# Kernel tuning notes

Hardware: AMD Instinct MI355X
Metric: run time of the kernel (lower is better)

## Reference

```python
import jax, jax.numpy as jnp
import numpy as np

WINDOW = 2048
STEP = WINDOW // 2                 # 1024
N_SAMPLES = 131072
N_COEFFS = WINDOW // 2 + 1         # 1025
N_FRAMES = N_SAMPLES // STEP       # 128
Z_DIM = 128
BATCH, N_EVENTS, IMP_SAMPLES = 64, 1, 4096
BASE_RES = 0.02
RES_RANGE = (1.0 - BASE_RES) * 0.99


def setup_inputs() -> dict:
    key = jax.random.key(0)
    k1, k2, k3 = jax.random.split(key, 3)
    z = jax.random.normal(k1, (BATCH, N_EVENTS, Z_DIM), dtype=jnp.float32)
    impulse = jax.random.normal(k2, (BATCH, N_EVENTS, IMP_SAMPLES), dtype=jnp.float32)
    # stand-in for ConvUpsample: linear z -> (n_coeffs * n_frames)
    W_tf = jax.random.normal(k3, (Z_DIM, N_COEFFS * N_FRAMES), dtype=jnp.float32) * 0.02
    b_tf = jnp.zeros((N_COEFFS * N_FRAMES,), dtype=jnp.float32)
    return {"z": z, "impulse": impulse, "W_tf": W_tf, "b_tf": b_tf}


def _hann(n):
    # periodic hann (torch.hann_window default)
    return (0.5 - 0.5 * jnp.cos(2.0 * jnp.pi * jnp.arange(n) / n)).astype(jnp.float32)


def reference(z, impulse, W_tf, b_tf):
    B, E, imp_len = impulse.shape
    pad = N_SAMPLES - imp_len + WINDOW
    x = jnp.pad(impulse, ((0, 0), (0, 0), (0, pad)))  # (B,E,n_samples+window)
    win = _hann(WINDOW)

    # windowed_audio: overlapping frames * hann window -> (B,E,F,W)
    idx = jnp.arange(N_FRAMES)[:, None] * STEP + jnp.arange(WINDOW)[None, :]
    windowed = x[..., idx] * win

    # transfer functions: linear, reshape (C,F) -> transpose to (F,C), squash
    tf = (z.reshape(-1, Z_DIM) @ W_tf + b_tf).reshape(B, E, N_COEFFS, N_FRAMES)
    tf = jnp.transpose(tf, (0, 1, 3, 2))                       # (B,E,F,C)
    tf = BASE_RES + jax.nn.sigmoid(tf) * RES_RANGE

    cur_specs = jnp.fft.rfft(windowed, axis=-1)                # (B,E,F,C) complex64

    # advance_one_frame rotation: [re,im] @ [[c,-s],[s,-c]]
    g = jnp.linspace(0.0, np.pi, N_COEFFS).astype(jnp.float32)
    c, s = jnp.cos(g), jnp.sin(g)

    def step(prev_audio, inp):
        cur_spec, tfi = inp
        ps = jnp.fft.rfft(prev_audio, axis=-1)
        re, im = ps.real, ps.imag
        rot = jax.lax.complex(re * c + im * s, -(re * s + im * c))
        spec = (cur_spec + rot) * tfi
        audio = jnp.fft.irfft(spec, n=WINDOW, axis=-1)
        return audio, audio

    xs = (jnp.moveaxis(cur_specs, 2, 0), jnp.moveaxis(tf, 2, 0))
    init = jnp.zeros((B, E, WINDOW), dtype=jnp.float32)  # i==0: zero prev spec
    _, frames = jax.lax.scan(step, init, xs)             # (F,B,E,W)
    frames = jnp.moveaxis(frames, 0, 2) * win            # overlap_add apply_window=True

    # overlap-add with hop = WINDOW//2, vectorized via half-frame reshapes
    first = frames[..., :STEP].reshape(B, E, N_FRAMES * STEP)
    second = frames[..., STEP:].reshape(B, E, N_FRAMES * STEP)
    out = jnp.zeros((B, E, (N_FRAMES + 1) * STEP), dtype=jnp.float32)
    out = out.at[..., : N_FRAMES * STEP].add(first)
    out = out.at[..., STEP:].add(second)
    return out[..., :N_SAMPLES]
```

## Files before the change

### kernel.cpp

```cpp
#include <hip/hip_runtime.h>

#define NB 64
#define ZDIM 128
#define NCOEF 1025
#define NFR 128
#define COLS 131200
#define WINSZ 2048
#define HALFW 1024
#define NSAMP 131072
#define IMPN 4096
#define NCHUNK 32
#define NCK 31

#define TF_OFF   0
#define TF_SZ    (NB*COLS)
#define TFT_OFF  (TF_OFF + TF_SZ)
#define TFT_SZ   (NB*NFR*NCOEF)
#define CUR_OFF  (TFT_OFF + TFT_SZ)
#define CUR_SZ   (NB*4*NCOEF*2)
#define CK_OFF   (CUR_OFF + CUR_SZ)
#define CK_SZ    (NCK*NB*NCOEF*2)
#define WINT_OFF (CK_OFF + CK_SZ)
#define WINT_SZ  (WINSZ)
#define TW_OFF   (WINT_OFF + WINT_SZ)
#define TW_SZ    (HALFW*2)

#define PHYS(i) ((i) ^ (((i) >> 5) & 3))

typedef short bf16x8 __attribute__((ext_vector_type(8)));
typedef float f32x4 __attribute__((ext_vector_type(4)));

__global__ __launch_bounds__(256) void init_tables(float* __restrict__ winT,
                                                   float2* __restrict__ twG) {
  int i = blockIdx.x * 256 + threadIdx.x;
  if (i < WINSZ) {
    winT[i] = 0.5f - 0.5f * cosf((float)(2.0 * 3.14159265358979323846 / 2048.0) * (float)i);
  }
  if (i < HALFW) {
    float ang = (float)(-2.0 * 3.14159265358979323846 / 2048.0) * (float)i;
    float sv, cv;
    sincosf(ang, &sv, &cv);
    twG[i] = make_float2(cv, sv);
  }
}

__device__ __forceinline__ short f2bf(float f) {
  unsigned u = __builtin_bit_cast(unsigned, f);
  u += 0x7FFFu + ((u >> 16) & 1u);
  return (short)(u >> 16);
}

__global__ __launch_bounds__(256) void tf_gemm_mfma(const float* __restrict__ z,
                                                    const float* __restrict__ W,
                                                    const float* __restrict__ bias,
                                                    float* __restrict__ tf) {
  int tid = threadIdx.x;
  int wave = tid >> 6, lane = tid & 63;
  int colw = blockIdx.x * 128 + wave * 32;
  int lr = lane & 15;
  int lk = (lane >> 4) * 8;
  int lq = (lane >> 4) * 4;

  float bv[2];
#pragma unroll
  for (int n = 0; n < 2; ++n) bv[n] = bias[colw + 16 * n + lr];

  f32x4 acc[4][2];
#pragma unroll
  for (int m = 0; m < 4; ++m)
#pragma unroll
    for (int n = 0; n < 2; ++n)
      acc[m][n] = f32x4{bv[n], bv[n], bv[n], bv[n]};

#pragma unroll
  for (int s = 0; s < 4; ++s) {
    int k0 = s * 32 + lk;
    bf16x8 afr[4];
#pragma unroll
    for (int m = 0; m < 4; ++m) {
      const float* zp = z + (size_t)(16 * m + lr) * ZDIM + k0;
      float4 z0 = *reinterpret_cast<const float4*>(zp);
      float4 z1 = *reinterpret_cast<const float4*>(zp + 4);
      afr[m] = bf16x8{f2bf(z0.x), f2bf(z0.y), f2bf(z0.z), f2bf(z0.w),
                      f2bf(z1.x), f2bf(z1.y), f2bf(z1.z), f2bf(z1.w)};
    }
    bf16x8 bfr[2];
#pragma unroll
    for (int n = 0; n < 2; ++n) {
      const float* wp = W + (size_t)k0 * COLS + colw + 16 * n + lr;
      bfr[n] = bf16x8{f2bf(wp[0 * (size_t)COLS]), f2bf(wp[1 * (size_t)COLS]),
                      f2bf(wp[2 * (size_t)COLS]), f2bf(wp[3 * (size_t)COLS]),
                      f2bf(wp[4 * (size_t)COLS]), f2bf(wp[5 * (size_t)COLS]),
                      f2bf(wp[6 * (size_t)COLS]), f2bf(wp[7 * (size_t)COLS])};
    }
#pragma unroll
    for (int m = 0; m < 4; ++m)
#pragma unroll
      for (int n = 0; n < 2; ++n)
        acc[m][n] = __builtin_amdgcn_mfma_f32_16x16x32_bf16(afr[m], bfr[n], acc[m][n], 0, 0, 0);
  }

  const float RESR = (1.0f - 0.02f) * 0.99f;
#pragma unroll
  for (int n = 0; n < 2; ++n) {
    int col = colw + 16 * n + lr;
#pragma unroll
    for (int m = 0; m < 4; ++m) {
      int rowb = 16 * m + lq;
#pragma unroll
      for (int r = 0; r < 4; ++r) {
        float x = acc[m][n][r];
        float sg = 1.0f / (1.0f + __expf(-x));
        tf[(size_t)(rowb + r) * COLS + col] = 0.02f + sg * RESR;
      }
    }
  }
}

static __device__ __forceinline__ void wg_fft2048(float* ar, float* ai,
                                                  float* br, float* bi,
                                                  const float2* tw,
                                                  float** outr, float** outi) {
  float *xr = ar, *xi = ai, *yr = br, *yi = bi;
  int m = 1;
  for (int s = 0; s < 11; ++s) {
    __syncthreads();
#pragma unroll
    for (int it = 0; it < 4; ++it) {
      int t = (int)threadIdx.x + it * 256;
      int jm = t & ~(m - 1);
      float x0r = xr[t], x0i = xi[t];
      float x1r = xr[t + 1024], x1i = xi[t + 1024];
      float2 w = tw[jm];
      float sr = x0r + x1r, si = x0i + x1i;
      float dr = x0r - x1r, di = x0i - x1i;
      float pr = dr * w.x - di * w.y;
      float pi = dr * w.y + di * w.x;
      yr[t + jm] = sr;      yi[t + jm] = si;
      yr[t + jm + m] = pr;  yi[t + jm + m] = pi;
    }
    float* t0 = xr; xr = yr; yr = t0;
    float* t1 = xi; xi = yi; yi = t1;
    m <<= 1;
  }
  __syncthreads();
  *outr = xr; *outi = xi;
}

__global__ __launch_bounds__(256) void fwd_fft_kernel(const float* __restrict__ imp,
                                                      const float* __restrict__ winT,
                                                      const float2* __restrict__ twG,
                                                      float2* __restrict__ cur) {
  __shared__ float b0r[WINSZ], b0i[WINSZ], b1r[WINSZ], b1i[WINSZ];
  __shared__ float2 tw[HALFW];
  int wg = blockIdx.x;
  int b = wg >> 2, f = wg & 3;
  int tid = threadIdx.x;

  for (int i = tid; i < HALFW; i += 256) tw[i] = twG[i];
  for (int w = tid; w < WINSZ; w += 256) {
    int s = f * HALFW + w;
    float v = (s < IMPN) ? imp[(size_t)b * IMPN + s] * winT[w] : 0.0f;
    b0r[w] = v;
    b0i[w] = 0.0f;
  }
  float *rr, *ri;
  wg_fft2048(b0r, b0i, b1r, b1i, tw, &rr, &ri);
  for (int k = tid; k < NCOEF; k += 256)
    cur[(size_t)wg * NCOEF + k] = make_float2(rr[k], ri[k]);
}

__global__ __launch_bounds__(256) void recur_ck_t(const float* __restrict__ tf,
                                                  const float2* __restrict__ cur,
                                                  float2* __restrict__ ckp,
                                                  float* __restrict__ tft) {
  int id = blockIdx.x * 256 + threadIdx.x;
  if (id >= NB * NCOEF) return;
  int b = id / NCOEF;
  int k = id - b * NCOEF;

  float g = 3.14159265358979323846f * (float)k / 1024.0f;
  float sg, cg;
  sincosf(g, &sg, &cg);
  bool herm = (k == 0) || (k == HALFW);

  const float4* tf4 = (const float4*)(tf + (size_t)b * COLS + (size_t)k * NFR);
  const float2* curb = cur + (size_t)b * 4 * NCOEF + k;
  float* tftb = tft + (size_t)b * NFR * NCOEF + k;

  float pre = 0.0f, pim = 0.0f;
  for (int f4 = 0; f4 < 32; ++f4) {
    float4 tv = tf4[f4];
    float tfs[4] = {tv.x, tv.y, tv.z, tv.w};
#pragma unroll
    for (int u = 0; u < 4; ++u) {
      int f = 4 * f4 + u;
      tftb[(size_t)f * NCOEF] = tfs[u];
      if (f < 124) {
        float tfv = tfs[u];
        float cr = 0.0f, ci = 0.0f;
        if (f < 4) {
          float2 cv = curb[(size_t)f * NCOEF];
          cr = cv.x; ci = cv.y;
        }
        float ire = herm ? 0.0f : pim;
        float rre = fmaf(pre, cg, ire * sg);
        float rim = -fmaf(pre, sg, ire * cg);
        float sre = (cr + rre) * tfv;
        float sim = (ci + rim) * tfv;
        if ((f & 3) == 2)
          ckp[(size_t)((f - 2) >> 2) * NB * NCOEF + (size_t)b * NCOEF + k] = make_float2(sre, sim);
        pre = sre; pim = sim;
      }
    }
  }
}

__global__ __launch_bounds__(256) void fused_resyn(const float* __restrict__ tft,
                                                   const float2* __restrict__ cur,
                                                   const float2* __restrict__ ckp,
                                                   const float* __restrict__ winT,
                                                   const float2* __restrict__ twG,
                                                   float* __restrict__ out) {
  __shared__ float L0r[1024], L0i[1024], L1r[1024], L1i[1024];
  __shared__ float2 twL[256];

  int bidx = blockIdx.x;
  int b = bidx >> 5, c = bidx & 31;
  int tid = threadIdx.x;

  twL[tid] = twG[2 * tid];

  float pre[5], pim[5], cgv[5], sgv[5];
#pragma unroll
  for (int i = 0; i < 5; ++i) {
    if (i == 4) { cgv[4] = -1.0f; sgv[4] = 0.0f; }
    else {
      float2 tv = twG[tid + 256 * i];
      cgv[i] = tv.x; sgv[i] = -tv.y;
    }
    pre[i] = 0.0f; pim[i] = 0.0f;
  }
  if (c > 0) {
    const float2* ck = ckp + ((size_t)(c - 1) * NB + b) * NCOEF;
#pragma unroll
    for (int i = 0; i < 5; ++i) {
      if (i == 4 && tid != 0) continue;
      int k = (i == 4) ? 1024 : tid + 256 * i;
      float2 v = ck[k];
      pre[i] = v.x; pim[i] = v.y;
    }
  }

  int fs = (c == 0) ? 0 : 4 * c - 1;
  int fe2 = 4 * c + 3;
  float ce0 = 0.0f, co0 = 0.0f, ce1 = 0.0f, co1 = 0.0f;
  const float* tftb = tft + (size_t)b * NFR * NCOEF;
  const float2* curb = cur + (size_t)b * 4 * NCOEF;
  const float2* win2 = (const float2*)winT;
  const float scale = 1.0f / 1024.0f;
  __syncthreads();

  for (int f = fs; f <= fe2; ++f) {
    const float* tfr = tftb + (size_t)f * NCOEF;
    float sreg[5], simg[5];
#pragma unroll
    for (int i = 0; i < 5; ++i) {
      if (i == 4 && tid != 0) { sreg[4] = 0.0f; simg[4] = 0.0f; continue; }
      int k = (i == 4) ? 1024 : tid + 256 * i;
      float tfv = tfr[k];
      float cr = 0.0f, ci = 0.0f;
      if (f < 4) {
        float2 cv = curb[(size_t)f * NCOEF + k];
        cr = cv.x; ci = cv.y;
      }
      float rre = fmaf(pre[i], cgv[i], pim[i] * sgv[i]);
      float rim = -fmaf(pre[i], sgv[i], pim[i] * cgv[i]);
      float sre = (cr + rre) * tfv;
      float sim = (ci + rim) * tfv;
      sreg[i] = sre; simg[i] = sim;
      pre[i] = sre; pim[i] = sim;
    }
    __syncthreads();
#pragma unroll
    for (int i = 0; i < 4; ++i) {
      int pk = PHYS(tid + 256 * i);
      L1r[pk] = sreg[i]; L1i[pk] = simg[i];
    }
    __syncthreads();
#pragma unroll
    for (int it = 0; it < 4; ++it) {
      int j = tid + it * 256;
      float2 tg = twG[j];
      float cc = tg.x, sn = -tg.y;
      int pj = PHYS(j);
      float xjr = L1r[pj], xji = L1i[pj];
      float xmr, xmi;
      if (j == 0) { xmr = sreg[4]; xmi = 0.0f; }
      else { int pm = PHYS(1024 - j); xmr = L1r[pm]; xmi = L1i[pm]; }
      float Xer = 0.5f * (xjr + xmr), Xei = 0.5f * (xji - xmi);
      float Xpr = 0.5f * (xjr - xmr), Xpi = 0.5f * (xji + xmi);
      float Xor_ = Xpr * cc - Xpi * sn;
      float Xoi_ = Xpr * sn + Xpi * cc;
      L0r[pj] = Xer - Xoi_;
      L0i[pj] = -(Xei + Xor_);
    }
    int t = tid;
#pragma unroll
    for (int st = 0; st < 5; ++st) {
      __syncthreads();
      int s = 1 << (2 * st);
      int q = t & (s - 1);
      int j = t & ~(s - 1);
      float2 w1 = twL[j];
      float w1x = w1.x, w1y = w1.y;
      float w2x = w1x * w1x - w1y * w1y, w2y = 2.0f * w1x * w1y;
      float w3x = w2x * w1x - w2y * w1y, w3y = w2x * w1y + w2y * w1x;
      int i0 = PHYS(t), i1 = PHYS(t + 256), i2 = PHYS(t + 512), i3 = PHYS(t + 768);
      int wb = (j << 2) + q;
      int o0 = PHYS(wb), o1 = PHYS(wb + s), o2 = PHYS(wb + 2 * s), o3 = PHYS(wb + 3 * s);
      const float *xr, *xi;
      float *yr, *yi;
      if (st & 1) { xr = L1r; xi = L1i; yr = L0r; yi = L0i; }
      else        { xr = L0r; xi = L0i; yr = L1r; yi = L1i; }
      float ar_ = xr[i0], ai_ = xi[i0];
      float br_ = xr[i1], bi_ = xi[i1];
      float cr_ = xr[i2], ci_ = xi[i2];
      float dr_ = xr[i3], di_ = xi[i3];
      float apcr = ar_ + cr_, apci = ai_ + ci_;
      float amcr = ar_ - cr_, amci = ai_ - ci_;
      float bpdr = br_ + dr_, bpdi = bi_ + di_;
      float bmdr = br_ - dr_, bmdi = bi_ - di_;
      yr[o0] = apcr + bpdr;             yi[o0] = apci + bpdi;
      float t1r = amcr + bmdi, t1i = amci - bmdr;
      yr[o1] = t1r * w1x - t1i * w1y;   yi[o1] = t1r * w1y + t1i * w1x;
      float t2r = apcr - bpdr, t2i = apci - bpdi;
      yr[o2] = t2r * w2x - t2i * w2y;   yi[o2] = t2r * w2y + t2i * w2x;
      float t3r = amcr - bmdi, t3i = amci + bmdr;
      yr[o3] = t3r * w3x - t3i * w3y;   yi[o3] = t3r * w3y + t3i * w3x;
    }
    __syncthreads();
#pragma unroll
    for (int it = 0; it < 2; ++it) {
      int mI = tid + it * 256;
      float2 wa = win2[mI];
      float2 wb2 = win2[mI + 512];
      int pa = PHYS(mI), pb = PHYS(mI + 512);
      float fe_ = L1r[pa] * scale * wa.x;
      float fo_ = -L1i[pa] * scale * wa.y;
      float se_ = L1r[pb] * scale * wb2.x;
      float so_ = -L1i[pb] * scale * wb2.y;
      if (f >= 4 * c) {
        float2* ob = (float2*)(out + (size_t)b * NSAMP + (size_t)f * 1024);
        float pce = it ? ce1 : ce0, pco = it ? co1 : co0;
        ob[mI] = make_float2(fe_ + pce, fo_ + pco);
      }
      if (it) { ce1 = se_; co1 = so_; } else { ce0 = se_; co0 = so_; }
    }
  }
}

extern "C" void kernel_launch(void* const* d_in, const int* in_sizes, int n_in,
                              void* d_out, int out_size, void* d_ws, size_t ws_size,
                              hipStream_t stream) {
  const float* z    = (const float*)d_in[0];
  const float* imp  = (const float*)d_in[1];
  const float* W    = (const float*)d_in[2];
  const float* bias = (const float*)d_in[3];

  float* ws = (float*)d_ws;
  float*  tf   = ws + TF_OFF;
  float*  tft  = ws + TFT_OFF;
  float2* cur  = (float2*)(ws + CUR_OFF);
  float2* ckp  = (float2*)(ws + CK_OFF);
  float*  winT = ws + WINT_OFF;
  float2* twG  = (float2*)(ws + TW_OFF);
  float*  out  = (float*)d_out;

  init_tables<<<8, 256, 0, stream>>>(winT, twG);
  tf_gemm_mfma<<<COLS / 128, 256, 0, stream>>>(z, W, bias, tf);
  fwd_fft_kernel<<<NB * 4, 256, 0, stream>>>(imp, winT, twG, cur);
  recur_ck_t<<<(NB * NCOEF + 255) / 256, 256, 0, stream>>>(tf, cur, ckp, tft);
  fused_resyn<<<NB * NCHUNK, 256, 0, stream>>>(tft, cur, ckp, winT, twG, out);
}
```

Measured before the change: 104.5 us.

## Process two frames per FFT pass with larger chunks and interleaved complex LDS

Halves the number of chunks per batch from 32 to 16, so each block handles 8 frames, and processes two frames per iteration. Their inverse FFTs share barriers and twiddle computation. Shared buffers become interleaved float2 arrays and the 1/1024 scale is folded into the pre-twiddle constant. This cuts barriers per frame and redundant warm-up frames, but halves the grid to 1024 blocks and raises register and LDS pressure.

```diff
diff --git a/kernel.cpp b/kernel.cpp
--- a/kernel.cpp
+++ b/kernel.cpp
@@ -9,8 +9,8 @@
 #define HALFW 1024
 #define NSAMP 131072
 #define IMPN 4096
-#define NCHUNK 32
-#define NCK 31
+#define NCHUNK 16
+#define NCK 15
 
 #define TF_OFF   0
 #define TF_SZ    (NB*COLS)
@@ -196,7 +196,7 @@
     for (int u = 0; u < 4; ++u) {
       int f = 4 * f4 + u;
       tftb[(size_t)f * NCOEF] = tfs[u];
-      if (f < 124) {
+      if (f < 120) {
         float tfv = tfs[u];
         float cr = 0.0f, ci = 0.0f;
         if (f < 4) {
@@ -208,8 +208,8 @@
         float rim = -fmaf(pre, sg, ire * cg);
         float sre = (cr + rre) * tfv;
         float sim = (ci + rim) * tfv;
-        if ((f & 3) == 2)
-          ckp[(size_t)((f - 2) >> 2) * NB * NCOEF + (size_t)b * NCOEF + k] = make_float2(sre, sim);
+        if ((f & 7) == 6)
+          ckp[(size_t)((f - 6) >> 3) * NB * NCOEF + (size_t)b * NCOEF + k] = make_float2(sre, sim);
         pre = sre; pim = sim;
       }
     }
@@ -222,13 +222,14 @@
                                                    const float* __restrict__ winT,
                                                    const float2* __restrict__ twG,
                                                    float* __restrict__ out) {
-  __shared__ float L0r[1024], L0i[1024], L1r[1024], L1i[1024];
+  __shared__ float2 PA0[1024], PB0[1024];
+  __shared__ float2 PA1[1024], PB1[1024];
   __shared__ float2 twL[256];
+  __shared__ float nyqv[2];
 
   int bidx = blockIdx.x;
-  int b = bidx >> 5, c = bidx & 31;
+  int b = bidx >> 4, c = bidx & 15;
   int tid = threadIdx.x;
-
   twL[tid] = twG[2 * tid];
 
   float pre[5], pim[5], cgv[5], sgv[5];
@@ -252,112 +253,152 @@
     }
   }
 
-  int fs = (c == 0) ? 0 : 4 * c - 1;
-  int fe2 = 4 * c + 3;
-  float ce0 = 0.0f, co0 = 0.0f, ce1 = 0.0f, co1 = 0.0f;
   const float* tftb = tft + (size_t)b * NFR * NCOEF;
   const float2* curb = cur + (size_t)b * 4 * NCOEF;
   const float2* win2 = (const float2*)winT;
-  const float scale = 1.0f / 1024.0f;
+  int fs = (c == 0) ? 0 : 8 * c - 1;
+  int fe = 8 * c + 7;
+  float ce[2] = {0.0f, 0.0f}, co[2] = {0.0f, 0.0f};
+
+#define ADVANCE(F, S, I)                                                     \
+  do {                                                                       \
+    const float* tfr_ = tftb + (size_t)(F) * NCOEF;                          \
+    _Pragma("unroll")                                                        \
+    for (int i_ = 0; i_ < 5; ++i_) {                                         \
+      if (i_ == 4 && tid != 0) { S[4] = 0.0f; I[4] = 0.0f; continue; }       \
+      int k_ = (i_ == 4) ? 1024 : tid + 256 * i_;                            \
+      float tfv_ = tfr_[k_];                                                 \
+      float cr_ = 0.0f, ci_ = 0.0f;                                          \
+      if ((F) < 4) {                                                         \
+        float2 cv_ = curb[(size_t)(F) * NCOEF + k_];                         \
+        cr_ = cv_.x; ci_ = cv_.y;                                            \
+      }                                                                      \
+      float rre_ = fmaf(pre[i_], cgv[i_], pim[i_] * sgv[i_]);                \
+      float rim_ = -fmaf(pre[i_], sgv[i_], pim[i_] * cgv[i_]);               \
+      S[i_] = (cr_ + rre_) * tfv_;                                           \
+      I[i_] = (ci_ + rim_) * tfv_;                                           \
+      pre[i_] = S[i_]; pim[i_] = I[i_];                                      \
+    }                                                                        \
+  } while (0)
+
   __syncthreads();
 
-  for (int f = fs; f <= fe2; ++f) {
-    const float* tfr = tftb + (size_t)f * NCOEF;
-    float sreg[5], simg[5];
-#pragma unroll
-    for (int i = 0; i < 5; ++i) {
-      if (i == 4 && tid != 0) { sreg[4] = 0.0f; simg[4] = 0.0f; continue; }
-      int k = (i == 4) ? 1024 : tid + 256 * i;
-      float tfv = tfr[k];
-      float cr = 0.0f, ci = 0.0f;
-      if (f < 4) {
-        float2 cv = curb[(size_t)f * NCOEF + k];
-        cr = cv.x; ci = cv.y;
-      }
-      float rre = fmaf(pre[i], cgv[i], pim[i] * sgv[i]);
-      float rim = -fmaf(pre[i], sgv[i], pim[i] * cgv[i]);
-      float sre = (cr + rre) * tfv;
-      float sim = (ci + rim) * tfv;
-      sreg[i] = sre; simg[i] = sim;
-      pre[i] = sre; pim[i] = sim;
-    }
+  for (int fA = fs; fA <= fe; fA += 2) {
+    int fB = fA + 1;
+    bool hasB = (fB <= fe);
+
+    float sA[5], iA[5], sB[5], iB[5];
+    ADVANCE(fA, sA, iA);
+    if (hasB) ADVANCE(fB, sB, iB);
+    else {
+#pragma unroll
+      for (int i = 0; i < 5; ++i) { sB[i] = 0.0f; iB[i] = 0.0f; }
+    }
+
     __syncthreads();
 #pragma unroll
     for (int i = 0; i < 4; ++i) {
       int pk = PHYS(tid + 256 * i);
-      L1r[pk] = sreg[i]; L1i[pk] = simg[i];
-    }
+      PA1[pk] = make_float2(sA[i], iA[i]);
+      PB1[pk] = make_float2(sB[i], iB[i]);
+    }
+    if (tid == 0) { nyqv[0] = sA[4]; nyqv[1] = sB[4]; }
     __syncthreads();
+
+    const float Cs = 0.5f / 1024.0f;
 #pragma unroll
     for (int it = 0; it < 4; ++it) {
       int j = tid + it * 256;
       float2 tg = twG[j];
       float cc = tg.x, sn = -tg.y;
       int pj = PHYS(j);
-      float xjr = L1r[pj], xji = L1i[pj];
-      float xmr, xmi;
-      if (j == 0) { xmr = sreg[4]; xmi = 0.0f; }
-      else { int pm = PHYS(1024 - j); xmr = L1r[pm]; xmi = L1i[pm]; }
-      float Xer = 0.5f * (xjr + xmr), Xei = 0.5f * (xji - xmi);
-      float Xpr = 0.5f * (xjr - xmr), Xpi = 0.5f * (xji + xmi);
-      float Xor_ = Xpr * cc - Xpi * sn;
-      float Xoi_ = Xpr * sn + Xpi * cc;
-      L0r[pj] = Xer - Xoi_;
-      L0i[pj] = -(Xei + Xor_);
-    }
-    int t = tid;
+      int pm = PHYS((HALFW - j) & 1023);
+      {
+        float2 xj = PA1[pj];
+        float xmr, xmi;
+        if (j == 0) { xmr = nyqv[0]; xmi = 0.0f; }
+        else { float2 xm = PA1[pm]; xmr = xm.x; xmi = xm.y; }
+        float Xer = Cs * (xj.x + xmr), Xei = Cs * (xj.y - xmi);
+        float Xpr = Cs * (xj.x - xmr), Xpi = Cs * (xj.y + xmi);
+        float Xor_ = Xpr * cc - Xpi * sn;
+        float Xoi_ = Xpr * sn + Xpi * cc;
+        PA0[pj] = make_float2(Xer - Xoi_, -(Xei + Xor_));
+      }
+      {
+        float2 xj = PB1[pj];
+        float xmr, xmi;
+        if (j == 0) { xmr = nyqv[1]; xmi = 0.0f; }
+        else { float2 xm = PB1[pm]; xmr = xm.x; xmi = xm.y; }
+        float Xer = Cs * (xj.x + xmr), Xei = Cs * (xj.y - xmi);
+        float Xpr = Cs * (xj.x - xmr), Xpi = Cs * (xj.y + xmi);
+        float Xor_ = Xpr * cc - Xpi * sn;
+        float Xoi_ = Xpr * sn + Xpi * cc;
+        PB0[pj] = make_float2(Xer - Xoi_, -(Xei + Xor_));
+      }
+    }
+
+    int i0 = PHYS(tid), i1 = PHYS(tid + 256), i2 = PHYS(tid + 512), i3 = PHYS(tid + 768);
 #pragma unroll
     for (int st = 0; st < 5; ++st) {
       __syncthreads();
       int s = 1 << (2 * st);
-      int q = t & (s - 1);
-      int j = t & ~(s - 1);
+      int q = tid & (s - 1);
+      int j = tid & ~(s - 1);
       float2 w1 = twL[j];
       float w1x = w1.x, w1y = w1.y;
       float w2x = w1x * w1x - w1y * w1y, w2y = 2.0f * w1x * w1y;
       float w3x = w2x * w1x - w2y * w1y, w3y = w2x * w1y + w2y * w1x;
-      int i0 = PHYS(t), i1 = PHYS(t + 256), i2 = PHYS(t + 512), i3 = PHYS(t + 768);
       int wb = (j << 2) + q;
       int o0 = PHYS(wb), o1 = PHYS(wb + s), o2 = PHYS(wb + 2 * s), o3 = PHYS(wb + 3 * s);
-      const float *xr, *xi;
-      float *yr, *yi;
-      if (st & 1) { xr = L1r; xi = L1i; yr = L0r; yi = L0i; }
-      else        { xr = L0r; xi = L0i; yr = L1r; yi = L1i; }
-      float ar_ = xr[i0], ai_ = xi[i0];
-      float br_ = xr[i1], bi_ = xi[i1];
-      float cr_ = xr[i2], ci_ = xi[i2];
-      float dr_ = xr[i3], di_ = xi[i3];
-      float apcr = ar_ + cr_, apci = ai_ + ci_;
-      float amcr = ar_ - cr_, amci = ai_ - ci_;
-      float bpdr = br_ + dr_, bpdi = bi_ + di_;
-      float bmdr = br_ - dr_, bmdi = bi_ - di_;
-      yr[o0] = apcr + bpdr;             yi[o0] = apci + bpdi;
-      float t1r = amcr + bmdi, t1i = amci - bmdr;
-      yr[o1] = t1r * w1x - t1i * w1y;   yi[o1] = t1r * w1y + t1i * w1x;
-      float t2r = apcr - bpdr, t2i = apci - bpdi;
-      yr[o2] = t2r * w2x - t2i * w2y;   yi[o2] = t2r * w2y + t2i * w2x;
-      float t3r = amcr - bmdi, t3i = amci + bmdr;
-      yr[o3] = t3r * w3x - t3i * w3y;   yi[o3] = t3r * w3y + t3i * w3x;
+      const float2 *xA, *xB;
+      float2 *yA, *yB;
+      if (st & 1) { xA = PA1; xB = PB1; yA = PA0; yB = PB0; }
+      else        { xA = PA0; xB = PB0; yA = PA1; yB = PB1; }
+
+#define BFLY4(X, Y)                                                          \
+      do {                                                                   \
+        float2 a_ = X[i0], b_ = X[i1], c_ = X[i2], d_ = X[i3];               \
+        float apcr = a_.x + c_.x, apci = a_.y + c_.y;                        \
+        float amcr = a_.x - c_.x, amci = a_.y - c_.y;                        \
+        float bpdr = b_.x + d_.x, bpdi = b_.y + d_.y;                        \
+        float bmdr = b_.x - d_.x, bmdi = b_.y - d_.y;                        \
+        Y[o0] = make_float2(apcr + bpdr, apci + bpdi);                       \
+        float t1r = amcr + bmdi, t1i = amci - bmdr;                          \
+        Y[o1] = make_float2(t1r * w1x - t1i * w1y, t1r * w1y + t1i * w1x);   \
+        float t2r = apcr - bpdr, t2i = apci - bpdi;                          \
+        Y[o2] = make_float2(t2r * w2x - t2i * w2y, t2r * w2y + t2i * w2x);   \
+        float t3r = amcr - bmdi, t3i = amci + bmdr;                          \
+        Y[o3] = make_float2(t3r * w3x - t3i * w3y, t3r * w3y + t3i * w3x);   \
+      } while (0)
+
+      BFLY4(xA, yA);
+      BFLY4(xB, yB);
+#undef BFLY4
     }
     __syncthreads();
+
 #pragma unroll
     for (int it = 0; it < 2; ++it) {
       int mI = tid + it * 256;
-      float2 wa = win2[mI];
-      float2 wb2 = win2[mI + 512];
       int pa = PHYS(mI), pb = PHYS(mI + 512);
-      float fe_ = L1r[pa] * scale * wa.x;
-      float fo_ = -L1i[pa] * scale * wa.y;
-      float se_ = L1r[pb] * scale * wb2.x;
-      float so_ = -L1i[pb] * scale * wb2.y;
-      if (f >= 4 * c) {
-        float2* ob = (float2*)(out + (size_t)b * NSAMP + (size_t)f * 1024);
-        float pce = it ? ce1 : ce0, pco = it ? co1 : co0;
-        ob[mI] = make_float2(fe_ + pce, fo_ + pco);
-      }
-      if (it) { ce1 = se_; co1 = so_; } else { ce0 = se_; co0 = so_; }
-    }
-  }
+      float2 wva = win2[mI], wvb = win2[mI + 512];
+      float2 a1 = PA1[pa], a2 = PA1[pb];
+      float fe_ = a1.x * wva.x, fo_ = -a1.y * wva.y;
+      if (fA >= 8 * c) {
+        float2* ob = (float2*)(out + (size_t)b * NSAMP + (size_t)fA * 1024);
+        ob[mI] = make_float2(fe_ + ce[it], fo_ + co[it]);
+      }
+      float nce = a2.x * wvb.x, nco = -a2.y * wvb.y;
+      if (hasB) {
+        float2 b1 = PB1[pa], b2 = PB1[pb];
+        float2* ob = (float2*)(out + (size_t)b * NSAMP + (size_t)fB * 1024);
+        ob[mI] = make_float2(b1.x * wva.x + nce, -b1.y * wva.y + nco);
+        nce = b2.x * wvb.x; nco = -b2.y * wvb.y;
+      }
+      ce[it] = nce; co[it] = nco;
+    }
+  }
+#undef ADVANCE
 }
 
 extern "C" void kernel_launch(void* const* d_in, const int* in_sizes, int n_in,
```

Result: faster. 102.4 us (-2.0%).

## Restructure in-block inverse FFT to use wave-local stages and fewer barriers

Applied to the files above, without the earlier changes.

Rewrites the per-frame 1024-point inverse complex FFT in fused_resyn. It now keeps interleaved float2 data in one shared buffer and does the pre-twiddle and first radix-4 stage in registers. The later stages are laid out so each wavefront only touches its own data, so s_waitcnt replaces most __syncthreads. Stage twiddles and window values are precomputed per thread outside the frame loop, and the final radix-4 stage writes results straight to output in digit-reversed order. This cuts block barriers, shared-memory traffic and global twiddle loads per frame, at the cost of relying on wave-local ordering assumptions and a new swizzle.

```diff
diff --git a/kernel.cpp b/kernel.cpp
--- a/kernel.cpp
+++ b/kernel.cpp
@@ -25,10 +25,14 @@
 #define TW_OFF   (WINT_OFF + WINT_SZ)
 #define TW_SZ    (HALFW*2)
 
-#define PHYS(i) ((i) ^ (((i) >> 5) & 3))
+#define PHI(p) ((p) ^ ((((p) >> 4) & 3) << 2))
 
 typedef short bf16x8 __attribute__((ext_vector_type(8)));
 typedef float f32x4 __attribute__((ext_vector_type(4)));
+
+__device__ __forceinline__ float2 cmul(float2 a, float2 b) {
+  return make_float2(a.x * b.x - a.y * b.y, a.x * b.y + a.y * b.x);
+}
 
 __global__ __launch_bounds__(256) void init_tables(float* __restrict__ winT,
                                                    float2* __restrict__ twG) {
@@ -222,21 +226,18 @@
                                                    const float* __restrict__ winT,
                                                    const float2* __restrict__ twG,
                                                    float* __restrict__ out) {
-  __shared__ float L0r[1024], L0i[1024], L1r[1024], L1i[1024];
-  __shared__ float2 twL[256];
+  __shared__ float2 P[1024];
 
   int bidx = blockIdx.x;
   int b = bidx >> 5, c = bidx & 31;
-  int tid = threadIdx.x;
-
-  twL[tid] = twG[2 * tid];
+  int t = threadIdx.x;
 
   float pre[5], pim[5], cgv[5], sgv[5];
 #pragma unroll
   for (int i = 0; i < 5; ++i) {
     if (i == 4) { cgv[4] = -1.0f; sgv[4] = 0.0f; }
     else {
-      float2 tv = twG[tid + 256 * i];
+      float2 tv = twG[t + 256 * i];
       cgv[i] = tv.x; sgv[i] = -tv.y;
     }
     pre[i] = 0.0f; pim[i] = 0.0f;
@@ -245,118 +246,176 @@
     const float2* ck = ckp + ((size_t)(c - 1) * NB + b) * NCOEF;
 #pragma unroll
     for (int i = 0; i < 5; ++i) {
-      if (i == 4 && tid != 0) continue;
-      int k = (i == 4) ? 1024 : tid + 256 * i;
+      if (i == 4 && t != 0) continue;
+      int k = (i == 4) ? 1024 : t + 256 * i;
       float2 v = ck[k];
       pre[i] = v.x; pim[i] = v.y;
     }
   }
 
-  int fs = (c == 0) ? 0 : 4 * c - 1;
-  int fe2 = 4 * c + 3;
-  float ce0 = 0.0f, co0 = 0.0f, ce1 = 0.0f, co1 = 0.0f;
+  float2 w1a = twG[2 * t];            float2 w1b = cmul(w1a, w1a); float2 w1c = cmul(w1b, w1a);
+  float2 w2a = twG[8 * (t & 63)];     float2 w2b = cmul(w2a, w2a); float2 w2c = cmul(w2b, w2a);
+  float2 w3a = twG[32 * (t & 15)];    float2 w3b = cmul(w3a, w3a); float2 w3c = cmul(w3b, w3a);
+  float2 w4a = twG[128 * (t & 3)];    float2 w4b = cmul(w4a, w4a); float2 w4c = cmul(w4b, w4a);
+  float2 twp0 = twG[t], twp1 = twG[t + 256], twp2 = twG[t + 512], twp3 = twG[t + 768];
+
+  int mb = (t >> 6) + ((t >> 4) & 3) * 4 + ((t >> 2) & 3) * 16 + (t & 3) * 64;
+  const float2* win2 = (const float2*)winT;
+  float2 wv0 = win2[mb], wv1 = win2[mb + 256], wv2 = win2[mb + 512], wv3 = win2[mb + 768];
+
+  int X0 = PHI(t);
+  int B2 = 256 * (t >> 6) + ((t & 63) ^ (((t >> 4) & 3) << 2));
+  int b3h = 64 * (t >> 4), i3 = t & 15;
+  int b4h = 16 * (t >> 2), i4 = t & 3, c4 = (t >> 2) & 3;
+  int p5 = b4h + 4 * ((t & 3) ^ c4);
+  int pm0 = PHI((1024 - t) & 1023);
+  int pm1 = PHI((1024 - (t + 256)) & 1023);
+  int pm2 = PHI((1024 - (t + 512)) & 1023);
+  int pm3 = PHI((1024 - (t + 768)) & 1023);
+
   const float* tftb = tft + (size_t)b * NFR * NCOEF;
   const float2* curb = cur + (size_t)b * 4 * NCOEF;
-  const float2* win2 = (const float2*)winT;
-  const float scale = 1.0f / 1024.0f;
-  __syncthreads();
-
-  for (int f = fs; f <= fe2; ++f) {
-    const float* tfr = tftb + (size_t)f * NCOEF;
-    float sreg[5], simg[5];
-#pragma unroll
-    for (int i = 0; i < 5; ++i) {
-      if (i == 4 && tid != 0) { sreg[4] = 0.0f; simg[4] = 0.0f; continue; }
-      int k = (i == 4) ? 1024 : tid + 256 * i;
-      float tfv = tfr[k];
-      float cr = 0.0f, ci = 0.0f;
-      if (f < 4) {
-        float2 cv = curb[(size_t)f * NCOEF + k];
-        cr = cv.x; ci = cv.y;
+  const float Cs = 0.5f / 1024.0f;
+
+  int fs = (c == 0) ? 0 : 4 * c - 1;
+  int fe = 4 * c + 3;
+  float carE0 = 0.0f, carO0 = 0.0f, carE1 = 0.0f, carO1 = 0.0f;
+
+  for (int f = fs; f <= fe; ++f) {
+    float S[5], I[5];
+    {
+      const float* tfr = tftb + (size_t)f * NCOEF;
+#pragma unroll
+      for (int i = 0; i < 5; ++i) {
+        if (i == 4 && t != 0) { S[4] = 0.0f; I[4] = 0.0f; continue; }
+        int k = (i == 4) ? 1024 : t + 256 * i;
+        float tfv = tfr[k];
+        float cr = 0.0f, ci = 0.0f;
+        if (f < 4) {
+          float2 cv = curb[(size_t)f * NCOEF + k];
+          cr = cv.x; ci = cv.y;
+        }
+        float rre = fmaf(pre[i], cgv[i], pim[i] * sgv[i]);
+        float rim = -fmaf(pre[i], sgv[i], pim[i] * cgv[i]);
+        S[i] = (cr + rre) * tfv;
+        I[i] = (ci + rim) * tfv;
+        pre[i] = S[i]; pim[i] = I[i];
       }
-      float rre = fmaf(pre[i], cgv[i], pim[i] * sgv[i]);
-      float rim = -fmaf(pre[i], sgv[i], pim[i] * cgv[i]);
-      float sre = (cr + rre) * tfv;
-      float sim = (ci + rim) * tfv;
-      sreg[i] = sre; simg[i] = sim;
-      pre[i] = sre; pim[i] = sim;
-    }
+    }
+
     __syncthreads();
 #pragma unroll
-    for (int i = 0; i < 4; ++i) {
-      int pk = PHYS(tid + 256 * i);
-      L1r[pk] = sreg[i]; L1i[pk] = simg[i];
-    }
+    for (int i = 0; i < 4; ++i)
+      P[X0 + 256 * i] = make_float2(S[i], I[i]);
     __syncthreads();
-#pragma unroll
-    for (int it = 0; it < 4; ++it) {
-      int j = tid + it * 256;
-      float2 tg = twG[j];
-      float cc = tg.x, sn = -tg.y;
-      int pj = PHYS(j);
-      float xjr = L1r[pj], xji = L1i[pj];
-      float xmr, xmi;
-      if (j == 0) { xmr = sreg[4]; xmi = 0.0f; }
-      else { int pm = PHYS(1024 - j); xmr = L1r[pm]; xmi = L1i[pm]; }
-      float Xer = 0.5f * (xjr + xmr), Xei = 0.5f * (xji - xmi);
-      float Xpr = 0.5f * (xjr - xmr), Xpi = 0.5f * (xji + xmi);
-      float Xor_ = Xpr * cc - Xpi * sn;
-      float Xoi_ = Xpr * sn + Xpi * cc;
-      L0r[pj] = Xer - Xoi_;
-      L0i[pj] = -(Xei + Xor_);
-    }
-    int t = tid;
-#pragma unroll
-    for (int st = 0; st < 5; ++st) {
-      __syncthreads();
-      int s = 1 << (2 * st);
-      int q = t & (s - 1);
-      int j = t & ~(s - 1);
-      float2 w1 = twL[j];
-      float w1x = w1.x, w1y = w1.y;
-      float w2x = w1x * w1x - w1y * w1y, w2y = 2.0f * w1x * w1y;
-      float w3x = w2x * w1x - w2y * w1y, w3y = w2x * w1y + w2y * w1x;
-      int i0 = PHYS(t), i1 = PHYS(t + 256), i2 = PHYS(t + 512), i3 = PHYS(t + 768);
-      int wb = (j << 2) + q;
-      int o0 = PHYS(wb), o1 = PHYS(wb + s), o2 = PHYS(wb + 2 * s), o3 = PHYS(wb + 3 * s);
-      const float *xr, *xi;
-      float *yr, *yi;
-      if (st & 1) { xr = L1r; xi = L1i; yr = L0r; yi = L0i; }
-      else        { xr = L0r; xi = L0i; yr = L1r; yi = L1i; }
-      float ar_ = xr[i0], ai_ = xi[i0];
-      float br_ = xr[i1], bi_ = xi[i1];
-      float cr_ = xr[i2], ci_ = xi[i2];
-      float dr_ = xr[i3], di_ = xi[i3];
-      float apcr = ar_ + cr_, apci = ai_ + ci_;
-      float amcr = ar_ - cr_, amci = ai_ - ci_;
-      float bpdr = br_ + dr_, bpdi = bi_ + di_;
-      float bmdr = br_ - dr_, bmdi = bi_ - di_;
-      yr[o0] = apcr + bpdr;             yi[o0] = apci + bpdi;
-      float t1r = amcr + bmdi, t1i = amci - bmdr;
-      yr[o1] = t1r * w1x - t1i * w1y;   yi[o1] = t1r * w1y + t1i * w1x;
-      float t2r = apcr - bpdr, t2i = apci - bpdi;
-      yr[o2] = t2r * w2x - t2i * w2y;   yi[o2] = t2r * w2y + t2i * w2x;
-      float t3r = amcr - bmdi, t3i = amci + bmdr;
-      yr[o3] = t3r * w3x - t3i * w3y;   yi[o3] = t3r * w3y + t3i * w3x;
+
+    float2 Z[4];
+    {
+      float2 xm[4];
+      xm[0] = (t == 0) ? make_float2(S[4], 0.0f) : P[pm0];
+      xm[1] = P[pm1]; xm[2] = P[pm2]; xm[3] = P[pm3];
+      float2 twp[4] = {twp0, twp1, twp2, twp3};
+#pragma unroll
+      for (int i = 0; i < 4; ++i) {
+        float xjr = S[i], xji = I[i];
+        float cc = twp[i].x, sn = -twp[i].y;
+        float Xer = Cs * (xjr + xm[i].x), Xei = Cs * (xji - xm[i].y);
+        float Xpr = Cs * (xjr - xm[i].x), Xpi = Cs * (xji + xm[i].y);
+        float Xor_ = Xpr * cc - Xpi * sn;
+        float Xoi_ = Xpr * sn + Xpi * cc;
+        Z[i] = make_float2(Xer - Xoi_, -(Xei + Xor_));
+      }
+    }
+    float2 y0, y1, y2, y3;
+    {
+      float2 A = make_float2(Z[0].x + Z[2].x, Z[0].y + Z[2].y);
+      float2 Bv = make_float2(Z[0].x - Z[2].x, Z[0].y - Z[2].y);
+      float2 Cv = make_float2(Z[1].x + Z[3].x, Z[1].y + Z[3].y);
+      float2 D = make_float2(Z[1].x - Z[3].x, Z[1].y - Z[3].y);
+      y0 = make_float2(A.x + Cv.x, A.y + Cv.y);
+      y1 = cmul(make_float2(Bv.x + D.y, Bv.y - D.x), w1a);
+      y2 = cmul(make_float2(A.x - Cv.x, A.y - Cv.y), w1b);
+      y3 = cmul(make_float2(Bv.x - D.y, Bv.y + D.x), w1c);
     }
     __syncthreads();
-#pragma unroll
-    for (int it = 0; it < 2; ++it) {
-      int mI = tid + it * 256;
-      float2 wa = win2[mI];
-      float2 wb2 = win2[mI + 512];
-      int pa = PHYS(mI), pb = PHYS(mI + 512);
-      float fe_ = L1r[pa] * scale * wa.x;
-      float fo_ = -L1i[pa] * scale * wa.y;
-      float se_ = L1r[pb] * scale * wb2.x;
-      float so_ = -L1i[pb] * scale * wb2.y;
-      if (f >= 4 * c) {
-        float2* ob = (float2*)(out + (size_t)b * NSAMP + (size_t)f * 1024);
-        float pce = it ? ce1 : ce0, pco = it ? co1 : co0;
-        ob[mI] = make_float2(fe_ + pce, fo_ + pco);
-      }
-      if (it) { ce1 = se_; co1 = so_; } else { ce0 = se_; co0 = so_; }
-    }
+    P[X0]       = y0;
+    P[X0 + 256] = y1;
+    P[X0 + 512] = y2;
+    P[X0 + 768] = y3;
+    __syncthreads();
+
+    float2 u0 = P[B2], u1 = P[B2 + 64], u2 = P[B2 + 128], u3 = P[B2 + 192];
+    {
+      float2 A = make_float2(u0.x + u2.x, u0.y + u2.y);
+      float2 Bv = make_float2(u0.x - u2.x, u0.y - u2.y);
+      float2 Cv = make_float2(u1.x + u3.x, u1.y + u3.y);
+      float2 D = make_float2(u1.x - u3.x, u1.y - u3.y);
+      P[B2]       = make_float2(A.x + Cv.x, A.y + Cv.y);
+      P[B2 + 64]  = cmul(make_float2(Bv.x + D.y, Bv.y - D.x), w2a);
+      P[B2 + 128] = cmul(make_float2(A.x - Cv.x, A.y - Cv.y), w2b);
+      P[B2 + 192] = cmul(make_float2(Bv.x - D.y, Bv.y + D.x), w2c);
+    }
+    asm volatile("s_waitcnt lgkmcnt(0)" ::: "memory");
+
+    u0 = P[b3h + i3];
+    u1 = P[b3h + 16 + (i3 ^ 4)];
+    u2 = P[b3h + 32 + (i3 ^ 8)];
+    u3 = P[b3h + 48 + (i3 ^ 12)];
+    {
+      float2 A = make_float2(u0.x + u2.x, u0.y + u2.y);
+      float2 Bv = make_float2(u0.x - u2.x, u0.y - u2.y);
+      float2 Cv = make_float2(u1.x + u3.x, u1.y + u3.y);
+      float2 D = make_float2(u1.x - u3.x, u1.y - u3.y);
+      P[b3h + i3]             = make_float2(A.x + Cv.x, A.y + Cv.y);
+      P[b3h + 16 + (i3 ^ 4)]  = cmul(make_float2(Bv.x + D.y, Bv.y - D.x), w3a);
+      P[b3h + 32 + (i3 ^ 8)]  = cmul(make_float2(A.x - Cv.x, A.y - Cv.y), w3b);
+      P[b3h + 48 + (i3 ^ 12)] = cmul(make_float2(Bv.x - D.y, Bv.y + D.x), w3c);
+    }
+    asm volatile("s_waitcnt lgkmcnt(0)" ::: "memory");
+
+    u0 = P[b4h + 4 * (0 ^ c4) + i4];
+    u1 = P[b4h + 4 * (1 ^ c4) + i4];
+    u2 = P[b4h + 4 * (2 ^ c4) + i4];
+    u3 = P[b4h + 4 * (3 ^ c4) + i4];
+    {
+      float2 A = make_float2(u0.x + u2.x, u0.y + u2.y);
+      float2 Bv = make_float2(u0.x - u2.x, u0.y - u2.y);
+      float2 Cv = make_float2(u1.x + u3.x, u1.y + u3.y);
+      float2 D = make_float2(u1.x - u3.x, u1.y - u3.y);
+      P[b4h + 4 * (0 ^ c4) + i4] = make_float2(A.x + Cv.x, A.y + Cv.y);
+      P[b4h + 4 * (1 ^ c4) + i4] = cmul(make_float2(Bv.x + D.y, Bv.y - D.x), w4a);
+      P[b4h + 4 * (2 ^ c4) + i4] = cmul(make_float2(A.x - Cv.x, A.y - Cv.y), w4b);
+      P[b4h + 4 * (3 ^ c4) + i4] = cmul(make_float2(Bv.x - D.y, Bv.y + D.x), w4c);
+    }
+    asm volatile("s_waitcnt lgkmcnt(0)" ::: "memory");
+
+    float4 q01 = *reinterpret_cast<const float4*>(&P[p5]);
+    float4 q23 = *reinterpret_cast<const float4*>(&P[p5 + 2]);
+    float2 z0, z1, z2, z3;
+    {
+      float2 a = make_float2(q01.x, q01.y), bq = make_float2(q01.z, q01.w);
+      float2 cq = make_float2(q23.x, q23.y), d = make_float2(q23.z, q23.w);
+      float2 A = make_float2(a.x + cq.x, a.y + cq.y);
+      float2 Bv = make_float2(a.x - cq.x, a.y - cq.y);
+      float2 Cv = make_float2(bq.x + d.x, bq.y + d.y);
+      float2 D = make_float2(bq.x - d.x, bq.y - d.y);
+      z0 = make_float2(A.x + Cv.x, A.y + Cv.y);
+      z1 = make_float2(Bv.x + D.y, Bv.y - D.x);
+      z2 = make_float2(A.x - Cv.x, A.y - Cv.y);
+      z3 = make_float2(Bv.x - D.y, Bv.y + D.x);
+    }
+
+    float e0 = z0.x * wv0.x, o0 = -z0.y * wv0.y;
+    float e1 = z1.x * wv1.x, o1 = -z1.y * wv1.y;
+    float e2 = z2.x * wv2.x, o2 = -z2.y * wv2.y;
+    float e3 = z3.x * wv3.x, o3 = -z3.y * wv3.y;
+    if (f >= 4 * c) {
+      float2* ob2 = (float2*)(out + (size_t)b * NSAMP + (size_t)f * 1024);
+      ob2[mb]       = make_float2(e0 + carE0, o0 + carO0);
+      ob2[mb + 256] = make_float2(e1 + carE1, o1 + carO1);
+    }
+    carE0 = e2; carO0 = o2;
+    carE1 = e3; carO1 = o3;
   }
 }
 
```

New measurement: 96.27 us. 1.09x faster.
